# Performance work log

Measured on AMD Instinct MI355X. Metric: run time of the kernel, lower is better.

Reference implementation:

```python
import jax, jax.numpy as jnp
import numpy as np

HID = 256
NUM_ENT = 100000
NUM_REL = 50
E = 320000  # edges per direction; edge_index has 2*E columns
BN_EPS = 1e-5


def setup_inputs() -> dict:
    key = jax.random.key(0)
    ks = jax.random.split(key, 10)
    x = jax.random.normal(ks[0], (NUM_ENT, HID), dtype=jnp.float32)
    edge_index = jax.random.randint(ks[1], (2, 2 * E), 0, NUM_ENT)
    edge_type = jax.random.randint(ks[2], (2 * E,), 0, NUM_REL)
    rel_embed = jax.random.normal(ks[3], (NUM_REL, HID), dtype=jnp.float32)
    # xavier_normal init: std = sqrt(2 / (fan_in + fan_out))
    w_std = (2.0 / (HID + HID)) ** 0.5
    w_loop = jax.random.normal(ks[4], (HID, HID), dtype=jnp.float32) * w_std
    w_in = jax.random.normal(ks[5], (HID, HID), dtype=jnp.float32) * w_std
    w_out = jax.random.normal(ks[6], (HID, HID), dtype=jnp.float32) * w_std
    w_rel = jax.random.normal(ks[7], (HID, HID), dtype=jnp.float32) * w_std
    loop_rel = jax.random.normal(ks[8], (1, HID), dtype=jnp.float32) * ((2.0 / (1 + HID)) ** 0.5)
    bn_weight = jnp.ones((HID,), dtype=jnp.float32)
    bn_bias = jnp.zeros((HID,), dtype=jnp.float32)
    return {
        "x": x, "edge_index": edge_index, "edge_type": edge_type,
        "rel_embed": rel_embed, "w_loop": w_loop, "w_in": w_in,
        "w_out": w_out, "w_rel": w_rel, "loop_rel": loop_rel,
        "bn_weight": bn_weight, "bn_bias": bn_bias,
    }


def _compute_norm(edge_index, num_ent):
    # symmetric D^-1/2 * D^-1/2 norm; degree counted on row (target) index
    row, col = edge_index[0], edge_index[1]
    deg = jax.ops.segment_sum(jnp.ones_like(row, dtype=jnp.float32), row, num_segments=num_ent)
    deg_inv = jnp.where(deg > 0, deg ** -0.5, 0.0)
    return deg_inv[row] * deg_inv[col]


def _propagate(x, idx, etype, rel_all, W, norm, num_ent):
    # gather source nodes (idx[1]), compose with relation emb (mult), transform, scale, scatter-add to targets (idx[0])
    msg = (x[idx[1]] * rel_all[etype]) @ W  # [E, d]
    if norm is not None:
        msg = msg * norm[:, None]
    return jax.ops.segment_sum(msg, idx[0], num_segments=num_ent)


def reference(x, edge_index, edge_type, rel_embed, w_loop, w_in, w_out, w_rel,
              loop_rel, bn_weight, bn_bias):
    num_ent = x.shape[0]
    rel_all = jnp.concatenate([rel_embed, loop_rel], axis=0)  # [R+1, d]
    e = edge_index.shape[1] // 2
    in_index, out_index = edge_index[:, :e], edge_index[:, e:]
    in_type, out_type = edge_type[:e], edge_type[e:]

    in_norm = _compute_norm(in_index, num_ent)
    out_norm = _compute_norm(out_index, num_ent)

    in_res = _propagate(x, in_index, in_type, rel_all, w_in, in_norm, num_ent)
    out_res = _propagate(x, out_index, out_type, rel_all, w_out, out_norm, num_ent)
    # self-loop: identity scatter -> just per-node compose+transform
    loop_res = (x * loop_rel) @ w_loop

    out = (in_res + out_res + loop_res) * (1.0 / 3.0)

    # BatchNorm1d in training mode (batch stats, biased variance)
    mean = out.mean(axis=0)
    var = out.var(axis=0)
    out = (out - mean) * jax.lax.rsqrt(var + BN_EPS) * bn_weight + bn_bias

    rel_out = (rel_all @ w_rel)[:-1]  # drop loop relation
    return out, rel_out
```

## Files before the change

### kernel.cpp

```cpp
#include <hip/hip_runtime.h>

#define HID     256
#define N_ENT   100000
#define TOT_E   640000
#define HALF_E  320000
#define NSEG    (2 * N_ENT)
#define BN_EPSF 1e-5f
#define SCAN_ELEMS 1024
#define NBLK_SCAN  ((NSEG + SCAN_ELEMS - 1) / SCAN_ELEMS)

typedef short bf16x8 __attribute__((ext_vector_type(8)));
typedef float f32x4  __attribute__((ext_vector_type(4)));

__device__ __forceinline__ short f2b(float f) {
    union { float f; unsigned u; } c; c.f = f;
    unsigned u = c.u;
    u += 0x7FFF + ((u >> 16) & 1);
    return (short)(u >> 16);
}

__global__ void hist_kernel(const int* __restrict__ ei, int* __restrict__ offs) {
    int j = blockIdx.x * 256 + threadIdx.x;
    if (j >= TOT_E) return;
    int seg = ei[j] + ((j < HALF_E) ? 0 : N_ENT);
    atomicAdd(&offs[seg], 1);
}

__global__ __launch_bounds__(256) void scan1(int* __restrict__ offs, int* __restrict__ bsums) {
    __shared__ int tsum[256];
    int b = blockIdx.x, t = threadIdx.x;
    int base = b * SCAN_ELEMS + t * 4;
    int v[4] = {0, 0, 0, 0};
    if (base + 3 < NSEG) {
        int4 lv = *(const int4*)(offs + base);
        v[0] = lv.x; v[1] = lv.y; v[2] = lv.z; v[3] = lv.w;
    } else {
        for (int i = 0; i < 4; ++i) if (base + i < NSEG) v[i] = offs[base + i];
    }
    tsum[t] = v[0] + v[1] + v[2] + v[3];
    __syncthreads();
    for (int d = 1; d < 256; d <<= 1) {
        int val = (t >= d) ? tsum[t - d] : 0;
        __syncthreads();
        tsum[t] += val;
        __syncthreads();
    }
    int run = (t == 0) ? 0 : tsum[t - 1];
    if (t == 255) bsums[b] = tsum[255];
    int w[4];
    for (int i = 0; i < 4; ++i) { w[i] = run; run += v[i]; }
    if (base + 3 < NSEG) *(int4*)(offs + base) = make_int4(w[0], w[1], w[2], w[3]);
    else for (int i = 0; i < 4; ++i) if (base + i < NSEG) offs[base + i] = w[i];
}

__global__ void scan2(int* __restrict__ bsums) {
    __shared__ int tmp[256];
    int t = threadIdx.x;
    int v = (t < NBLK_SCAN) ? bsums[t] : 0;
    tmp[t] = v;
    __syncthreads();
    for (int d = 1; d < 256; d <<= 1) {
        int val = (t >= d) ? tmp[t - d] : 0;
        __syncthreads();
        tmp[t] += val;
        __syncthreads();
    }
    if (t < NBLK_SCAN) bsums[t] = (t == 0) ? 0 : tmp[t - 1];
}

__global__ __launch_bounds__(256) void scan3(int* __restrict__ offs, const int* __restrict__ bsums) {
    int b = blockIdx.x;
    int add = bsums[b];
    int base = b * SCAN_ELEMS + threadIdx.x * 4;
    if (base + 3 < NSEG) {
        int4 v = *(int4*)(offs + base);
        v.x += add; v.y += add; v.z += add; v.w += add;
        *(int4*)(offs + base) = v;
    } else {
        for (int i = 0; i < 4; ++i) if (base + i < NSEG) offs[base + i] += add;
    }
}

__global__ void fill_kernel(const int* __restrict__ ei, const int* __restrict__ et,
                            int* __restrict__ offs, int* __restrict__ elist) {
    int j = blockIdx.x * 256 + threadIdx.x;
    if (j >= TOT_E) return;
    int seg = ei[j] + ((j < HALF_E) ? 0 : N_ENT);
    int pos = atomicAdd(&offs[seg], 1);
    elist[pos] = ei[TOT_E + j] | (et[j] << 17);
}

__global__ __launch_bounds__(256) void gather_kernel(
        const float* __restrict__ x, const float* __restrict__ rel,
        const int* __restrict__ offs, const int* __restrict__ elist,
        float* __restrict__ accA, float* __restrict__ accB) {
    int s = blockIdx.x * 4 + (threadIdx.x >> 6);
    int lane = threadIdx.x & 63;
    int start = (s == 0) ? 0 : offs[s - 1];
    int end   = offs[s];
    int half_base = (s >= N_ENT) ? N_ENT : 0;
    int r = s - half_base;
    float4 a = make_float4(0.f, 0.f, 0.f, 0.f);
    if (end > start) {
        float inv_r = rsqrtf((float)(end - start));
        for (int e = start; e < end; ++e) {
            int p = elist[e];
            int c = p & 0x1FFFF;
            int t = p >> 17;
            int sc = half_base + c;
            int cs = (sc == 0) ? 0 : offs[sc - 1];
            int ce = offs[sc];
            if (ce > cs) {
                float norm = inv_r * rsqrtf((float)(ce - cs));
                float4 xv = *(const float4*)(x   + (size_t)c * HID + lane * 4);
                float4 rv = *(const float4*)(rel + (size_t)t * HID + lane * 4);
                a.x += xv.x * rv.x * norm;
                a.y += xv.y * rv.y * norm;
                a.z += xv.z * rv.z * norm;
                a.w += xv.w * rv.w * norm;
            }
        }
    }
    float* dst = ((s >= N_ENT) ? accB : accA) + (size_t)r * HID + lane * 4;
    *(float4*)dst = a;
}

__global__ void wcat_kernel(const float* __restrict__ w_in, const float* __restrict__ w_out,
                            const float* __restrict__ w_loop, const float* __restrict__ loop_rel,
                            short* __restrict__ WT) {
    int n = blockIdx.x;
    int t = threadIdx.x;
    float v0 = w_in  [(size_t)t * HID + n];
    float v1 = w_out [(size_t)t * HID + n];
    float v2 = w_loop[(size_t)t * HID + n] * loop_rel[t];
    short* row = WT + (size_t)n * 768;
    row[t]       = f2b(v0);
    row[256 + t] = f2b(v1);
    row[512 + t] = f2b(v2);
}

__global__ __launch_bounds__(256) void gemm_mfma(
        const float* __restrict__ accA, const float* __restrict__ accB,
        const float* __restrict__ x, const short* __restrict__ WT,
        float* __restrict__ out, float* __restrict__ stats)
{
    __shared__ __align__(16) short As[64 * 64];
    __shared__ __align__(16) short Bs[256 * 64];
    const int tid = threadIdx.x;
    const int l   = tid & 63;
    const int wid = tid >> 6;
    const int r0  = blockIdx.x * 64;
    const int lr  = l & 15;
    const int lg  = l >> 4;

    f32x4 acc[4][4];
    #pragma unroll
    for (int i = 0; i < 4; ++i)
        #pragma unroll
        for (int j = 0; j < 4; ++j)
            acc[i][j] = (f32x4){0.f, 0.f, 0.f, 0.f};

    const int sg = tid & 7;
    const int sr = tid >> 3;

    for (int kt = 0; kt < 12; ++kt) {
        const int src = kt >> 2;
        const float* Ap = (src == 0) ? accA : ((src == 1) ? accB : x);
        const int ksg = kt * 64;
        const int ksl = (kt & 3) * 64;
        __syncthreads();
        #pragma unroll
        for (int h = 0; h < 2; ++h) {
            int r  = sr + 32 * h;
            int gr = r0 + r;
            float4 v0 = make_float4(0.f,0.f,0.f,0.f), v1 = v0;
            if (gr < N_ENT) {
                const float* p = Ap + (size_t)gr * HID + ksl + sg * 8;
                v0 = *(const float4*)p;
                v1 = *(const float4*)(p + 4);
            }
            bf16x8 pk;
            pk[0]=f2b(v0.x); pk[1]=f2b(v0.y); pk[2]=f2b(v0.z); pk[3]=f2b(v0.w);
            pk[4]=f2b(v1.x); pk[5]=f2b(v1.y); pk[6]=f2b(v1.z); pk[7]=f2b(v1.w);
            *(bf16x8*)&As[r * 64 + (sg ^ (r & 7)) * 8] = pk;
        }
        #pragma unroll
        for (int i = 0; i < 8; ++i) {
            int n = sr + 32 * i;
            bf16x8 w = *(const bf16x8*)(WT + (size_t)n * 768 + ksg + sg * 8);
            *(bf16x8*)&Bs[n * 64 + (sg ^ (n & 7)) * 8] = w;
        }
        __syncthreads();
        #pragma unroll
        for (int kc = 0; kc < 2; ++kc) {
            const int gsel = kc * 4 + lg;
            bf16x8 af[4], bfr[4];
            #pragma unroll
            for (int i = 0; i < 4; ++i) {
                int r = 16 * i + lr;
                af[i] = *(const bf16x8*)&As[r * 64 + (gsel ^ (r & 7)) * 8];
            }
            #pragma unroll
            for (int j = 0; j < 4; ++j) {
                int n = wid * 64 + 16 * j + lr;
                bfr[j] = *(const bf16x8*)&Bs[n * 64 + (gsel ^ (n & 7)) * 8];
            }
            #pragma unroll
            for (int i = 0; i < 4; ++i)
                #pragma unroll
                for (int j = 0; j < 4; ++j)
                    acc[i][j] = __builtin_amdgcn_mfma_f32_16x16x32_bf16(
                                    af[i], bfr[j], acc[i][j], 0, 0, 0);
        }
    }

    const float third = 1.f / 3.f;
    float s[4]  = {0.f, 0.f, 0.f, 0.f};
    float sq[4] = {0.f, 0.f, 0.f, 0.f};
    #pragma unroll
    for (int i = 0; i < 4; ++i) {
        #pragma unroll
        for (int v = 0; v < 4; ++v) {
            int grow = r0 + 16 * i + lg * 4 + v;
            if (grow < N_ENT) {
                #pragma unroll
                for (int j = 0; j < 4; ++j) {
                    float val = acc[i][j][v] * third;
                    out[(size_t)grow * HID + wid * 64 + 16 * j + lr] = val;
                    s[j] += val; sq[j] += val * val;
                }
            }
        }
    }
    #pragma unroll
    for (int j = 0; j < 4; ++j) {
        s[j]  += __shfl_xor(s[j], 16);  s[j]  += __shfl_xor(s[j], 32);
        sq[j] += __shfl_xor(sq[j], 16); sq[j] += __shfl_xor(sq[j], 32);
    }
    if (lg == 0) {
        #pragma unroll
        for (int j = 0; j < 4; ++j) {
            int c = wid * 64 + 16 * j + lr;
            atomicAdd(&stats[c], s[j]);
            atomicAdd(&stats[HID + c], sq[j]);
        }
    }
}

__global__ void bn_apply(float* __restrict__ out, const float* __restrict__ stats,
                         const float* __restrict__ bnw, const float* __restrict__ bnb) {
    const float invN = 1.f / (float)N_ENT;
    const size_t total = (size_t)N_ENT * HID;
    for (size_t idx = (size_t)blockIdx.x * 256 + threadIdx.x; idx < total;
         idx += (size_t)gridDim.x * 256) {
        int c = (int)(idx & (HID - 1));
        float mean = stats[c] * invN;
        float var  = stats[HID + c] * invN - mean * mean;
        out[idx] = (out[idx] - mean) * rsqrtf(var + BN_EPSF) * bnw[c] + bnb[c];
    }
}

__global__ void relout_kernel(const float* __restrict__ rel_embed,
                              const float* __restrict__ w_rel,
                              float* __restrict__ rel_out) {
    __shared__ float row[HID];
    int r = blockIdx.x;
    int c = threadIdx.x;
    row[c] = rel_embed[(size_t)r * HID + c];
    __syncthreads();
    float s = 0.f;
    for (int k = 0; k < HID; ++k) s += row[k] * w_rel[(size_t)k * HID + c];
    rel_out[(size_t)r * HID + c] = s;
}

extern "C" void kernel_launch(void* const* d_in, const int* in_sizes, int n_in,
                              void* d_out, int out_size, void* d_ws, size_t ws_size,
                              hipStream_t stream) {
    const float* x        = (const float*)d_in[0];
    const int*   ei       = (const int*)d_in[1];
    const int*   et       = (const int*)d_in[2];
    const float* rel      = (const float*)d_in[3];
    const float* w_loop   = (const float*)d_in[4];
    const float* w_in     = (const float*)d_in[5];
    const float* w_out    = (const float*)d_in[6];
    const float* w_rel    = (const float*)d_in[7];
    const float* loop_rel = (const float*)d_in[8];
    const float* bnw      = (const float*)d_in[9];
    const float* bnb      = (const float*)d_in[10];

    float* out     = (float*)d_out;
    float* rel_out = out + (size_t)N_ENT * HID;
    float* accA    = out;
    float* accB    = (float*)d_ws;

    int*   offs  = (int*)(accB + (size_t)N_ENT * HID);
    int*   elist = offs + NSEG;
    short* WT    = (short*)elist;
    int*   bsums = elist + TOT_E;
    float* stats = (float*)(bsums + 256);

    hipMemsetAsync(offs, 0, NSEG * sizeof(int), stream);
    hipMemsetAsync(stats, 0, 512 * sizeof(float), stream);

    hist_kernel<<<TOT_E / 256, 256, 0, stream>>>(ei, offs);
    scan1<<<NBLK_SCAN, 256, 0, stream>>>(offs, bsums);
    scan2<<<1, 256, 0, stream>>>(bsums);
    scan3<<<NBLK_SCAN, 256, 0, stream>>>(offs, bsums);
    fill_kernel<<<TOT_E / 256, 256, 0, stream>>>(ei, et, offs, elist);
    gather_kernel<<<NSEG / 4, 256, 0, stream>>>(x, rel, offs, elist, accA, accB);
    wcat_kernel<<<256, 256, 0, stream>>>(w_in, w_out, w_loop, loop_rel, WT);
    gemm_mfma<<<(N_ENT + 63) / 64, 256, 0, stream>>>(accA, accB, x, WT, out, stats);
    bn_apply<<<2048, 256, 0, stream>>>(out, stats, bnw, bnb);
    relout_kernel<<<50, 256, 0, stream>>>(rel, w_rel, rel_out);
}
```

Measured before the change: 375.8 us.

## Convert x and accumulators to bf16, precompute per-edge norms, vectorize BN

Adds a workspace-size-gated path that converts x and relation embeddings to bf16 up front. The gather now reads bf16 rows and writes bf16 aggregates, and the GEMM consumes bf16 directly instead of converting fp32 on load. Per-edge symmetric norms are precomputed into an 8-byte edge list, and the gather loop is unrolled by two. BatchNorm apply is vectorized to float4 with a fused scale and shift. This halves gather and GEMM input traffic in exchange for an extra conversion pass over x, more workspace, and reduced precision of the intermediate sums.

```diff
diff --git a/kernel.cpp b/kernel.cpp
--- a/kernel.cpp
+++ b/kernel.cpp
@@ -10,6 +10,7 @@
 #define NBLK_SCAN  ((NSEG + SCAN_ELEMS - 1) / SCAN_ELEMS)
 
 typedef short bf16x8 __attribute__((ext_vector_type(8)));
+typedef short bf16x4 __attribute__((ext_vector_type(4)));
 typedef float f32x4  __attribute__((ext_vector_type(4)));
 
 __device__ __forceinline__ short f2b(float f) {
@@ -18,12 +19,24 @@
     u += 0x7FFF + ((u >> 16) & 1);
     return (short)(u >> 16);
 }
+__device__ __forceinline__ float b2f(short b) {
+    union { unsigned u; float f; } c;
+    c.u = ((unsigned)(unsigned short)b) << 16;
+    return c.f;
+}
 
 __global__ void hist_kernel(const int* __restrict__ ei, int* __restrict__ offs) {
     int j = blockIdx.x * 256 + threadIdx.x;
     if (j >= TOT_E) return;
     int seg = ei[j] + ((j < HALF_E) ? 0 : N_ENT);
     atomicAdd(&offs[seg], 1);
+}
+
+__global__ void rnorm_kernel(const int* __restrict__ offs, float* __restrict__ rnorm) {
+    int s = blockIdx.x * 256 + threadIdx.x;
+    if (s >= NSEG) return;
+    int c = offs[s];
+    rnorm[s] = (c > 0) ? rsqrtf((float)c) : 0.f;
 }
 
 __global__ __launch_bounds__(256) void scan1(int* __restrict__ offs, int* __restrict__ bsums) {
@@ -81,6 +94,19 @@
     }
 }
 
+__global__ void fill8_kernel(const int* __restrict__ ei, const int* __restrict__ et,
+                             int* __restrict__ offs, const float* __restrict__ rnorm,
+                             int2* __restrict__ elist8) {
+    int j = blockIdx.x * 256 + threadIdx.x;
+    if (j >= TOT_E) return;
+    int hb  = (j < HALF_E) ? 0 : N_ENT;
+    int seg = ei[j] + hb;
+    int col = ei[TOT_E + j];
+    float norm = rnorm[seg] * rnorm[hb + col];
+    int pos = atomicAdd(&offs[seg], 1);
+    elist8[pos] = make_int2(col | (et[j] << 17), __float_as_int(norm));
+}
+
 __global__ void fill_kernel(const int* __restrict__ ei, const int* __restrict__ et,
                             int* __restrict__ offs, int* __restrict__ elist) {
     int j = blockIdx.x * 256 + threadIdx.x;
@@ -88,6 +114,67 @@
     int seg = ei[j] + ((j < HALF_E) ? 0 : N_ENT);
     int pos = atomicAdd(&offs[seg], 1);
     elist[pos] = ei[TOT_E + j] | (et[j] << 17);
+}
+
+__global__ void tobf16_kernel(const float* __restrict__ src, short* __restrict__ dst, int n8) {
+    int i = blockIdx.x * 256 + threadIdx.x;
+    if (i >= n8) return;
+    const float4* p = (const float4*)(src + (size_t)i * 8);
+    float4 v0 = p[0], v1 = p[1];
+    bf16x8 pk;
+    pk[0]=f2b(v0.x); pk[1]=f2b(v0.y); pk[2]=f2b(v0.z); pk[3]=f2b(v0.w);
+    pk[4]=f2b(v1.x); pk[5]=f2b(v1.y); pk[6]=f2b(v1.z); pk[7]=f2b(v1.w);
+    *(bf16x8*)(dst + (size_t)i * 8) = pk;
+}
+
+__global__ __launch_bounds__(256) void gather_h(
+        const short* __restrict__ xh, const short* __restrict__ relh,
+        const int* __restrict__ offs, const int2* __restrict__ elist8,
+        short* __restrict__ accA, short* __restrict__ accB) {
+    int s = blockIdx.x * 4 + (threadIdx.x >> 6);
+    int lane = threadIdx.x & 63;
+    int start = (s == 0) ? 0 : offs[s - 1];
+    int end   = offs[s];
+    float ax0=0.f, ay0=0.f, az0=0.f, aw0=0.f;
+    float ax1=0.f, ay1=0.f, az1=0.f, aw1=0.f;
+    int e = start;
+    for (; e + 2 <= end; e += 2) {
+        int2 p0 = elist8[e];
+        int2 p1 = elist8[e + 1];
+        int   c0 = p0.x & 0x1FFFF, t0 = p0.x >> 17;
+        float n0 = __int_as_float(p0.y);
+        int   c1 = p1.x & 0x1FFFF, t1 = p1.x >> 17;
+        float n1 = __int_as_float(p1.y);
+        bf16x4 xv0 = *(const bf16x4*)(xh   + (size_t)c0 * HID + lane * 4);
+        bf16x4 rv0 = *(const bf16x4*)(relh + (size_t)t0 * HID + lane * 4);
+        bf16x4 xv1 = *(const bf16x4*)(xh   + (size_t)c1 * HID + lane * 4);
+        bf16x4 rv1 = *(const bf16x4*)(relh + (size_t)t1 * HID + lane * 4);
+        ax0 += b2f(xv0[0]) * b2f(rv0[0]) * n0;
+        ay0 += b2f(xv0[1]) * b2f(rv0[1]) * n0;
+        az0 += b2f(xv0[2]) * b2f(rv0[2]) * n0;
+        aw0 += b2f(xv0[3]) * b2f(rv0[3]) * n0;
+        ax1 += b2f(xv1[0]) * b2f(rv1[0]) * n1;
+        ay1 += b2f(xv1[1]) * b2f(rv1[1]) * n1;
+        az1 += b2f(xv1[2]) * b2f(rv1[2]) * n1;
+        aw1 += b2f(xv1[3]) * b2f(rv1[3]) * n1;
+    }
+    if (e < end) {
+        int2 p = elist8[e];
+        int   c = p.x & 0x1FFFF, t = p.x >> 17;
+        float n = __int_as_float(p.y);
+        bf16x4 xv = *(const bf16x4*)(xh   + (size_t)c * HID + lane * 4);
+        bf16x4 rv = *(const bf16x4*)(relh + (size_t)t * HID + lane * 4);
+        ax0 += b2f(xv[0]) * b2f(rv[0]) * n;
+        ay0 += b2f(xv[1]) * b2f(rv[1]) * n;
+        az0 += b2f(xv[2]) * b2f(rv[2]) * n;
+        aw0 += b2f(xv[3]) * b2f(rv[3]) * n;
+    }
+    int hb = (s >= N_ENT) ? N_ENT : 0;
+    short* dst = ((s >= N_ENT) ? accB : accA) + (size_t)(s - hb) * HID + lane * 4;
+    bf16x4 pk;
+    pk[0] = f2b(ax0 + ax1); pk[1] = f2b(ay0 + ay1);
+    pk[2] = f2b(az0 + az1); pk[3] = f2b(aw0 + aw1);
+    *(bf16x4*)dst = pk;
 }
 
 __global__ __launch_bounds__(256) void gather_kernel(
@@ -139,6 +226,107 @@
     row[512 + t] = f2b(v2);
 }
 
+__global__ __launch_bounds__(256) void gemm_mfma_h(
+        const short* __restrict__ accA, const short* __restrict__ accB,
+        const short* __restrict__ xh, const short* __restrict__ WT,
+        float* __restrict__ out, float* __restrict__ stats)
+{
+    __shared__ __align__(16) short As[64 * 64];
+    __shared__ __align__(16) short Bs[256 * 64];
+    const int tid = threadIdx.x;
+    const int l   = tid & 63;
+    const int wid = tid >> 6;
+    const int r0  = blockIdx.x * 64;
+    const int lr  = l & 15;
+    const int lg  = l >> 4;
+
+    f32x4 acc[4][4];
+    #pragma unroll
+    for (int i = 0; i < 4; ++i)
+        #pragma unroll
+        for (int j = 0; j < 4; ++j)
+            acc[i][j] = (f32x4){0.f, 0.f, 0.f, 0.f};
+
+    const int sg = tid & 7;
+    const int sr = tid >> 3;
+
+    for (int kt = 0; kt < 12; ++kt) {
+        const int src = kt >> 2;
+        const short* Ap = (src == 0) ? accA : ((src == 1) ? accB : xh);
+        const int ksg = kt * 64;
+        const int ksl = (kt & 3) * 64;
+        __syncthreads();
+        #pragma unroll
+        for (int h = 0; h < 2; ++h) {
+            int r  = sr + 32 * h;
+            int gr = r0 + r;
+            bf16x8 v = {0,0,0,0,0,0,0,0};
+            if (gr < N_ENT) v = *(const bf16x8*)(Ap + (size_t)gr * HID + ksl + sg * 8);
+            *(bf16x8*)&As[r * 64 + (sg ^ (r & 7)) * 8] = v;
+        }
+        #pragma unroll
+        for (int i = 0; i < 8; ++i) {
+            int n = sr + 32 * i;
+            bf16x8 w = *(const bf16x8*)(WT + (size_t)n * 768 + ksg + sg * 8);
+            *(bf16x8*)&Bs[n * 64 + (sg ^ (n & 7)) * 8] = w;
+        }
+        __syncthreads();
+        #pragma unroll
+        for (int kc = 0; kc < 2; ++kc) {
+            const int gsel = kc * 4 + lg;
+            bf16x8 af[4], bfr[4];
+            #pragma unroll
+            for (int i = 0; i < 4; ++i) {
+                int r = 16 * i + lr;
+                af[i] = *(const bf16x8*)&As[r * 64 + (gsel ^ (r & 7)) * 8];
+            }
+            #pragma unroll
+            for (int j = 0; j < 4; ++j) {
+                int n = wid * 64 + 16 * j + lr;
+                bfr[j] = *(const bf16x8*)&Bs[n * 64 + (gsel ^ (n & 7)) * 8];
+            }
+            #pragma unroll
+            for (int i = 0; i < 4; ++i)
+                #pragma unroll
+                for (int j = 0; j < 4; ++j)
+                    acc[i][j] = __builtin_amdgcn_mfma_f32_16x16x32_bf16(
+                                    af[i], bfr[j], acc[i][j], 0, 0, 0);
+        }
+    }
+
+    const float third = 1.f / 3.f;
+    float s[4]  = {0.f, 0.f, 0.f, 0.f};
+    float sq[4] = {0.f, 0.f, 0.f, 0.f};
+    #pragma unroll
+    for (int i = 0; i < 4; ++i) {
+        #pragma unroll
+        for (int v = 0; v < 4; ++v) {
+            int grow = r0 + 16 * i + lg * 4 + v;
+            if (grow < N_ENT) {
+                #pragma unroll
+                for (int j = 0; j < 4; ++j) {
+                    float val = acc[i][j][v] * third;
+                    out[(size_t)grow * HID + wid * 64 + 16 * j + lr] = val;
+                    s[j] += val; sq[j] += val * val;
+                }
+            }
+        }
+    }
+    #pragma unroll
+    for (int j = 0; j < 4; ++j) {
+        s[j]  += __shfl_xor(s[j], 16);  s[j]  += __shfl_xor(s[j], 32);
+        sq[j] += __shfl_xor(sq[j], 16); sq[j] += __shfl_xor(sq[j], 32);
+    }
+    if (lg == 0) {
+        #pragma unroll
+        for (int j = 0; j < 4; ++j) {
+            int c = wid * 64 + 16 * j + lr;
+            atomicAdd(&stats[c], s[j]);
+            atomicAdd(&stats[HID + c], sq[j]);
+        }
+    }
+}
+
 __global__ __launch_bounds__(256) void gemm_mfma(
         const float* __restrict__ accA, const float* __restrict__ accB,
         const float* __restrict__ x, const short* __restrict__ WT,
@@ -250,13 +438,20 @@
 __global__ void bn_apply(float* __restrict__ out, const float* __restrict__ stats,
                          const float* __restrict__ bnw, const float* __restrict__ bnb) {
     const float invN = 1.f / (float)N_ENT;
-    const size_t total = (size_t)N_ENT * HID;
-    for (size_t idx = (size_t)blockIdx.x * 256 + threadIdx.x; idx < total;
-         idx += (size_t)gridDim.x * 256) {
-        int c = (int)(idx & (HID - 1));
-        float mean = stats[c] * invN;
-        float var  = stats[HID + c] * invN - mean * mean;
-        out[idx] = (out[idx] - mean) * rsqrtf(var + BN_EPSF) * bnw[c] + bnb[c];
+    const int total4 = N_ENT * (HID / 4);
+    for (int i = blockIdx.x * 256 + threadIdx.x; i < total4; i += gridDim.x * 256) {
+        int c = (i & 63) * 4;
+        float4 v = *(float4*)(out + (size_t)i * 4);
+        #pragma unroll
+        for (int k = 0; k < 4; ++k) {
+            float mean = stats[c + k] * invN;
+            float var  = stats[HID + c + k] * invN - mean * mean;
+            float sc   = rsqrtf(var + BN_EPSF) * bnw[c + k];
+            float sh   = bnb[c + k] - mean * sc;
+            float* comp = (k == 0) ? &v.x : (k == 1) ? &v.y : (k == 2) ? &v.z : &v.w;
+            *comp = (*comp) * sc + sh;
+        }
+        *(float4*)(out + (size_t)i * 4) = v;
     }
 }
 
@@ -290,26 +485,64 @@
 
     float* out     = (float*)d_out;
     float* rel_out = out + (size_t)N_ENT * HID;
-    float* accA    = out;
-    float* accB    = (float*)d_ws;
-
-    int*   offs  = (int*)(accB + (size_t)N_ENT * HID);
-    int*   elist = offs + NSEG;
-    short* WT    = (short*)elist;
-    int*   bsums = elist + TOT_E;
-    float* stats = (float*)(bsums + 256);
-
-    hipMemsetAsync(offs, 0, NSEG * sizeof(int), stream);
-    hipMemsetAsync(stats, 0, 512 * sizeof(float), stream);
-
-    hist_kernel<<<TOT_E / 256, 256, 0, stream>>>(ei, offs);
-    scan1<<<NBLK_SCAN, 256, 0, stream>>>(offs, bsums);
-    scan2<<<1, 256, 0, stream>>>(bsums);
-    scan3<<<NBLK_SCAN, 256, 0, stream>>>(offs, bsums);
-    fill_kernel<<<TOT_E / 256, 256, 0, stream>>>(ei, et, offs, elist);
-    gather_kernel<<<NSEG / 4, 256, 0, stream>>>(x, rel, offs, elist, accA, accB);
-    wcat_kernel<<<256, 256, 0, stream>>>(w_in, w_out, w_loop, loop_rel, WT);
-    gemm_mfma<<<(N_ENT + 63) / 64, 256, 0, stream>>>(accA, accB, x, WT, out, stats);
-    bn_apply<<<2048, 256, 0, stream>>>(out, stats, bnw, bnb);
-    relout_kernel<<<50, 256, 0, stream>>>(rel, w_rel, rel_out);
-}
+
+    const size_t XH_B   = (size_t)N_ENT * HID * 2;
+    const size_t ACC_B  = (size_t)N_ENT * HID * 2;
+    const size_t OFFS_B = (size_t)NSEG * 4;
+    const size_t EL8_B  = (size_t)TOT_E * 8;
+    const size_t RN_B   = (size_t)NSEG * 4;
+    const size_t need_big = XH_B + 2 * ACC_B + OFFS_B + EL8_B + RN_B
+                          + 256 * 4 + 512 * 4 + (size_t)50 * HID * 2;
+
+    if (ws_size >= need_big) {
+        char* w = (char*)d_ws;
+        short* xh     = (short*)w;              w += XH_B;
+        short* accA_h = (short*)w;              w += ACC_B;
+        short* accB_h = (short*)w;              w += ACC_B;
+        int*   offs   = (int*)w;                w += OFFS_B;
+        int2*  elist8 = (int2*)w;               short* WT = (short*)w;   w += EL8_B;
+        float* rnorm  = (float*)w;              w += RN_B;
+        int*   bsums  = (int*)w;                w += 256 * 4;
+        float* stats  = (float*)w;              w += 512 * 4;
+        short* relh   = (short*)w;
+
+        hipMemsetAsync(offs, 0, OFFS_B, stream);
+        hipMemsetAsync(stats, 0, 512 * 4, stream);
+
+        tobf16_kernel<<<(N_ENT * HID / 8 + 255) / 256, 256, 0, stream>>>(x, xh, N_ENT * HID / 8);
+        tobf16_kernel<<<(50 * HID / 8 + 255) / 256, 256, 0, stream>>>(rel, relh, 50 * HID / 8);
+        hist_kernel<<<TOT_E / 256, 256, 0, stream>>>(ei, offs);
+        rnorm_kernel<<<(NSEG + 255) / 256, 256, 0, stream>>>(offs, rnorm);
+        scan1<<<NBLK_SCAN, 256, 0, stream>>>(offs, bsums);
+        scan2<<<1, 256, 0, stream>>>(bsums);
+        scan3<<<NBLK_SCAN, 256, 0, stream>>>(offs, bsums);
+        fill8_kernel<<<TOT_E / 256, 256, 0, stream>>>(ei, et, offs, rnorm, elist8);
+        gather_h<<<NSEG / 4, 256, 0, stream>>>(xh, relh, offs, elist8, accA_h, accB_h);
+        wcat_kernel<<<256, 256, 0, stream>>>(w_in, w_out, w_loop, loop_rel, WT);
+        gemm_mfma_h<<<(N_ENT + 63) / 64, 256, 0, stream>>>(accA_h, accB_h, xh, WT, out, stats);
+        bn_apply<<<2048, 256, 0, stream>>>(out, stats, bnw, bnb);
+        relout_kernel<<<50, 256, 0, stream>>>(rel, w_rel, rel_out);
+    } else {
+        float* accA    = out;
+        float* accB    = (float*)d_ws;
+        int*   offs  = (int*)(accB + (size_t)N_ENT * HID);
+        int*   elist = offs + NSEG;
+        short* WT    = (short*)elist;
+        int*   bsums = elist + TOT_E;
+        float* stats = (float*)(bsums + 256);
+
+        hipMemsetAsync(offs, 0, NSEG * sizeof(int), stream);
+        hipMemsetAsync(stats, 0, 512 * sizeof(float), stream);
+
+        hist_kernel<<<TOT_E / 256, 256, 0, stream>>>(ei, offs);
+        scan1<<<NBLK_SCAN, 256, 0, stream>>>(offs, bsums);
+        scan2<<<1, 256, 0, stream>>>(bsums);
+        scan3<<<NBLK_SCAN, 256, 0, stream>>>(offs, bsums);
+        fill_kernel<<<TOT_E / 256, 256, 0, stream>>>(ei, et, offs, elist);
+        gather_kernel<<<NSEG / 4, 256, 0, stream>>>(x, rel, offs, elist, accA, accB);
+        wcat_kernel<<<256, 256, 0, stream>>>(w_in, w_out, w_loop, loop_rel, WT);
+        gemm_mfma<<<(N_ENT + 63) / 64, 256, 0, stream>>>(accA, accB, x, WT, out, stats);
+        bn_apply<<<2048, 256, 0, stream>>>(out, stats, bnw, bnb);
+        relout_kernel<<<50, 256, 0, stream>>>(rel, w_rel, rel_out);
+    }
+}
```

Result: faster. 315.8 us (-16.0%).
